# Performance work log

Measured on AMD Instinct MI355X. Metric: run time of the kernel, lower is better.

The kernel has to match this reference:

```python
import jax, jax.numpy as jnp
import numpy as np

ALPHA = 0.2  # LeakyReLU negative slope
NEG_INF = -9e15


def setup_inputs() -> dict:
    key = jax.random.key(0)
    k1, k2, k3, k4 = jax.random.split(key, 4)
    B, N, F_in, F_out = 8, 2048, 256, 128
    h = jax.random.normal(k1, (B, N, F_in), dtype=jnp.float32)
    adj = jax.random.randint(k2, (B, N, N), 0, 2, dtype=jnp.int32)
    # xavier_uniform with gain=1.414
    def xavier(k, shape, gain=1.414):
        fan_in, fan_out = shape[0], shape[1]
        limit = gain * np.sqrt(6.0 / (fan_in + fan_out))
        return jax.random.uniform(k, shape, jnp.float32, -limit, limit)
    W = xavier(k3, (F_in, F_out))
    a = xavier(k4, (2 * F_out, 1))
    return {"h": h, "adj": adj, "W": W, "a": a}


def reference(h, adj, W, a):
    # h: [B,N,F_in], adj: [B,N,N], W: [F_in,F_out], a: [2*F_out,1]
    Wh = jnp.einsum('bnf,fe->bne', h, W)  # [B,N,E]
    E = Wh.shape[-1]
    a_src, a_dst = a[:E, 0], a[E:, 0]
    # e[b,i,j] = leakyrelu(Wh[b,i].a_src + Wh[b,j].a_dst)  (additive decomposition
    # of a @ concat(Wh_i, Wh_j) -- same math, no [B,N,N,2E] intermediate)
    s_src = Wh @ a_src  # [B,N]
    s_dst = Wh @ a_dst  # [B,N]
    e = jax.nn.leaky_relu(s_src[:, :, None] + s_dst[:, None, :], negative_slope=ALPHA)
    e = jnp.where(adj > 0, e, NEG_INF)
    attention = jax.nn.softmax(e, axis=2)  # [B,N,N]
    # dropout p=0.0 / eval mode -> identity
    h_prime = jnp.einsum('bij,bje->bie', attention, Wh)
    return jax.nn.elu(h_prime)  # concat=True
```

## Files before the change

kernel.cpp:

```cpp
#include <hip/hip_runtime.h>
#include <hip/hip_bf16.h>

#define GAT_ALPHA 0.2f
#define LOG2E 1.4426950408889634f

typedef float f32x4 __attribute__((ext_vector_type(4)));
typedef int   i32x4 __attribute__((ext_vector_type(4)));
typedef short bf16x8 __attribute__((ext_vector_type(8)));

static constexpr int Nn  = 2048;
static constexpr int FIN = 256;
static constexpr int FO  = 128;

static __device__ __forceinline__ unsigned short f2bf(float x) {
    __hip_bfloat16 h = __float2bfloat16(x);
    return __builtin_bit_cast(unsigned short, h);
}
static __device__ __forceinline__ float bf2f(unsigned short u) {
    unsigned int v = ((unsigned int)u) << 16;
    return __builtin_bit_cast(float, v);
}

__global__ __launch_bounds__(256) void gat_prep(
        const float* __restrict__ W, const float* __restrict__ a,
        float* __restrict__ wa, unsigned int* __restrict__ md_key)
{
    __shared__ float pr[32][8];
    __shared__ float pd[32][8];
    const int t = threadIdx.x;
    const int kl = t >> 3, seg = t & 7;
    const int k = blockIdx.x * 32 + kl;
    float ps = 0.f, pv = 0.f;
    const float* wr = W + (size_t)k * FO + seg * 16;
    #pragma unroll
    for (int f = 0; f < 16; f += 4) {
        f32x4 wv = *(const f32x4*)(wr + f);
        f32x4 as = *(const f32x4*)(a + seg * 16 + f);
        f32x4 ad = *(const f32x4*)(a + FO + seg * 16 + f);
        ps += wv[0]*as[0] + wv[1]*as[1] + wv[2]*as[2] + wv[3]*as[3];
        pv += wv[0]*ad[0] + wv[1]*ad[1] + wv[2]*ad[2] + wv[3]*ad[3];
    }
    pr[kl][seg] = ps; pd[kl][seg] = pv;
    __syncthreads();
    if (t < 32) {
        float s = 0.f, d = 0.f;
        #pragma unroll
        for (int j = 0; j < 8; ++j) { s += pr[t][j]; d += pd[t][j]; }
        wa[blockIdx.x * 32 + t]       = s;
        wa[256 + blockIdx.x * 32 + t] = d;
    }
    if (blockIdx.x == 0 && t < 8) md_key[t] = 0u;
}

__global__ __launch_bounds__(256) void gat_wh(
        const float* __restrict__ h, const float* __restrict__ W,
        const float* __restrict__ wa, unsigned short* __restrict__ Wp,
        float* __restrict__ s_src, float* __restrict__ s_dst,
        unsigned int* __restrict__ md_key)
{
    __shared__ unsigned short WT[FO][264];
    __shared__ float wal[512];
    __shared__ float sred[64][4][2];
    __shared__ float red64[64];
    const int t  = threadIdx.x;
    const int b  = blockIdx.x & 7;
    const int n0 = (blockIdx.x >> 3) << 6;

    if (t < 128) *(f32x4*)&wal[t * 4] = *(const f32x4*)&wa[t * 4];
    #pragma unroll
    for (int c = 0; c < 32; ++c) {
        int flat = c * 1024 + t * 4;
        int k = flat >> 7, f = flat & 127;
        f32x4 wv = *(const f32x4*)&W[flat];
        WT[f + 0][k] = f2bf(wv[0]);
        WT[f + 1][k] = f2bf(wv[1]);
        WT[f + 2][k] = f2bf(wv[2]);
        WT[f + 3][k] = f2bf(wv[3]);
    }
    __syncthreads();

    {
        const int row = t >> 2, seg = t & 3;
        const float* hp  = h + ((size_t)(b * Nn + n0 + row)) * FIN + seg * 64;
        const float* was = &wal[seg * 64];
        const float* wad = &wal[256 + seg * 64];
        float ps = 0.f, pv = 0.f;
        #pragma unroll
        for (int j = 0; j < 64; j += 4) {
            f32x4 hv = *(const f32x4*)(hp + j);
            f32x4 sv = *(const f32x4*)(was + j);
            f32x4 dv = *(const f32x4*)(wad + j);
            ps += hv[0]*sv[0] + hv[1]*sv[1] + hv[2]*sv[2] + hv[3]*sv[3];
            pv += hv[0]*dv[0] + hv[1]*dv[1] + hv[2]*dv[2] + hv[3]*dv[3];
        }
        sred[row][seg][0] = ps;
        sred[row][seg][1] = pv;
    }
    __syncthreads();
    if (t < 64) {
        float s = sred[t][0][0] + sred[t][1][0] + sred[t][2][0] + sred[t][3][0];
        float d = sred[t][0][1] + sred[t][1][1] + sred[t][2][1] + sred[t][3][1];
        s_src[b * Nn + n0 + t] = s;
        s_dst[b * Nn + n0 + t] = d;
        red64[t] = d;
    }
    __syncthreads();
    if (t < 16) red64[t] = fmaxf(fmaxf(red64[t], red64[t + 16]),
                                 fmaxf(red64[t + 32], red64[t + 48]));
    __syncthreads();
    if (t == 0) {
        float m = red64[0];
        #pragma unroll
        for (int j = 1; j < 16; ++j) m = fmaxf(m, red64[j]);
        unsigned int bits = __builtin_bit_cast(unsigned int, m);
        unsigned int key  = (bits & 0x80000000u) ? ~bits : (bits | 0x80000000u);
        atomicMax(md_key + b, key);
    }

    const int w = t >> 6, lane = t & 63, n16 = lane & 15, quad = lane >> 4;
    const float* ha = h + ((size_t)(b * Nn + n0 + w * 16 + n16)) * FIN + quad * 8;
    f32x4 acc[8] = {};
    #pragma unroll
    for (int ks = 0; ks < 8; ++ks) {
        f32x4 h0 = *(const f32x4*)(ha + ks * 32);
        f32x4 h1 = *(const f32x4*)(ha + ks * 32 + 4);
        bf16x8 af;
        af[0] = (short)f2bf(h0[0]); af[1] = (short)f2bf(h0[1]);
        af[2] = (short)f2bf(h0[2]); af[3] = (short)f2bf(h0[3]);
        af[4] = (short)f2bf(h1[0]); af[5] = (short)f2bf(h1[1]);
        af[6] = (short)f2bf(h1[2]); af[7] = (short)f2bf(h1[3]);
        #pragma unroll
        for (int nt = 0; nt < 8; ++nt) {
            bf16x8 bfr = *(const bf16x8*)&WT[nt * 16 + n16][ks * 32 + quad * 8];
            acc[nt] = __builtin_amdgcn_mfma_f32_16x16x32_bf16(af, bfr, acc[nt], 0, 0, 0);
        }
    }
    {
        const int v      = (n0 >> 5) + (w >> 1);
        const int quad_p = ((w & 1) << 1) + (quad >> 1);
        const int eoff   = (quad & 1) << 2;
        #pragma unroll
        for (int nt = 0; nt < 8; ++nt) {
            ushort4 pk;
            pk.x = f2bf(acc[nt][0]); pk.y = f2bf(acc[nt][1]);
            pk.z = f2bf(acc[nt][2]); pk.w = f2bf(acc[nt][3]);
            size_t idx = ((((size_t)(b << 6) + v) * 8 + nt) * 64 + quad_p * 16 + n16) * 8 + eoff;
            *(ushort4*)&Wp[idx] = pk;
        }
    }
}

__global__ __launch_bounds__(512, 2) void gat_attn(
        const int* __restrict__ adj, const unsigned short* __restrict__ Wp,
        const float* __restrict__ s_src, const float* __restrict__ s_dst,
        const unsigned int* __restrict__ md_key, float* __restrict__ out)
{
    constexpr int AS = 132;
    __shared__ __align__(16) float smem_f[64 * AS];
    __shared__ float l_red[64];
    unsigned short* ldsw = (unsigned short*)smem_f;

    const int t = threadIdx.x, w = t >> 6, lane = t & 63;
    const int n16 = lane & 15, quad = lane >> 4;
    const int rg = w & 3, jwin = w >> 2;
    const int b  = blockIdx.x & 7;
    const int i0 = (blockIdx.x >> 3) << 6;

    if (t < 64) l_red[t] = 0.f;

    const unsigned int key = md_key[b];
    const unsigned int mb  = (key & 0x80000000u) ? (key ^ 0x80000000u) : ~key;
    const float mdb = __builtin_bit_cast(float, mb);

    const int row = i0 + rg * 16 + n16;
    const float ssr = s_src[b * Nn + row];
    const float tm  = ssr + mdb;
    const float mi  = fmaxf(tm, GAT_ALPHA * tm) * LOG2E;
    const float sL  = ssr * LOG2E;

    const int jw = (jwin << 5) + (quad << 3);
    const int* ap    = adj + ((size_t)(b * Nn + row)) * Nn + jw;
    const float* dptr = s_dst + b * Nn + jw;
    const unsigned short* wsrc = Wp + ((size_t)b << 18) + (t << 4);

    f32x4 acc[8] = {};
    float ls = 0.f;

    {
        f32x4 g0 = *(const f32x4*)(wsrc);
        f32x4 g1 = *(const f32x4*)(wsrc + 8);
        *(f32x4*)&ldsw[(t << 4)]     = g0;
        *(f32x4*)&ldsw[(t << 4) + 8] = g1;
    }
    i32x4 pa0 = *(const i32x4*)(ap);
    i32x4 pa1 = *(const i32x4*)(ap + 4);
    __syncthreads();

    for (int s = 0; s < 32; ++s) {
        const int j0  = s << 6;
        const int cur = s & 1, nxt = cur ^ 1;
        f32x4 d0 = *(const f32x4*)(dptr + j0);
        f32x4 d1 = *(const f32x4*)(dptr + j0 + 4);
        f32x4 g0, g1;
        if (s < 31) {
            const unsigned short* src = wsrc + (s + 1) * 8192;
            g0 = *(const f32x4*)(src);
            g1 = *(const f32x4*)(src + 8);
        }
        const int jn = (s < 31) ? ((s + 1) << 6) : 0;
        i32x4 na0 = *(const i32x4*)(ap + jn);
        i32x4 na1 = *(const i32x4*)(ap + jn + 4);

        bf16x8 af;
        #pragma unroll
        for (int j = 0; j < 4; ++j) {
            float u  = __builtin_fmaf(d0[j], LOG2E, sL);
            float lr = fmaxf(u, GAT_ALPHA * u);
            float e  = __builtin_amdgcn_exp2f(lr - mi);
            e = (pa0[j] > 0) ? e : 0.f;
            unsigned short us = f2bf(e);
            ls += bf2f(us); af[j] = (short)us;
        }
        #pragma unroll
        for (int j = 0; j < 4; ++j) {
            float u  = __builtin_fmaf(d1[j], LOG2E, sL);
            float lr = fmaxf(u, GAT_ALPHA * u);
            float e  = __builtin_amdgcn_exp2f(lr - mi);
            e = (pa1[j] > 0) ? e : 0.f;
            unsigned short us = f2bf(e);
            ls += bf2f(us); af[4 + j] = (short)us;
        }

        const unsigned short* bbase = &ldsw[cur * 8192 + (jwin << 12) + (lane << 3)];
        #pragma unroll
        for (int nt = 0; nt < 8; ++nt) {
            bf16x8 bfr = *(const bf16x8*)(bbase + (nt << 9));
            acc[nt] = __builtin_amdgcn_mfma_f32_16x16x32_bf16(af, bfr, acc[nt], 0, 0, 0);
        }

        if (s < 31) {
            *(f32x4*)&ldsw[nxt * 8192 + (t << 4)]     = g0;
            *(f32x4*)&ldsw[nxt * 8192 + (t << 4) + 8] = g1;
        }
        pa0 = na0; pa1 = na1;
        __syncthreads();
    }

    ls += __shfl_xor(ls, 16); ls += __shfl_xor(ls, 32);
    if (quad == 0) atomicAdd(&l_red[rg * 16 + n16], ls);

    float* slotp = smem_f + (size_t)(rg * 16) * AS;
    if (jwin == 0) {
        #pragma unroll
        for (int nt = 0; nt < 8; ++nt)
            #pragma unroll
            for (int rr = 0; rr < 4; ++rr)
                slotp[(quad * 4 + rr) * AS + nt * 16 + n16] = acc[nt][rr];
    }
    __syncthreads();
    if (jwin == 1) {
        #pragma unroll
        for (int nt = 0; nt < 8; ++nt)
            #pragma unroll
            for (int rr = 0; rr < 4; ++rr)
                slotp[(quad * 4 + rr) * AS + nt * 16 + n16] += acc[nt][rr];
    }
    __syncthreads();

    float* ob = out + ((size_t)(b * Nn + i0)) * FO;
    #pragma unroll
    for (int c = 0; c < 4; ++c) {
        int flat = c * 2048 + t * 4;
        int m = flat >> 7, f = flat & 127;
        f32x4 v = *(const f32x4*)&smem_f[(size_t)m * AS + f];
        float l = l_red[m];
        f32x4 o;
        #pragma unroll
        for (int j = 0; j < 4; ++j) {
            float x = v[j] / l;
            o[j] = x > 0.f ? x : expm1f(x);
        }
        *(f32x4*)&ob[(size_t)m * FO + f] = o;
    }
}

extern "C" void kernel_launch(void* const* d_in, const int* in_sizes, int n_in,
                              void* d_out, int out_size, void* d_ws, size_t ws_size,
                              hipStream_t stream)
{
    const float* h   = (const float*)d_in[0];
    const int*   adj = (const int*)d_in[1];
    const float* W   = (const float*)d_in[2];
    const float* a   = (const float*)d_in[3];
    float* out = (float*)d_out;

    char* ws = (char*)d_ws;
    unsigned short* Wp  = (unsigned short*)ws;
    float* s_src        = (float*)(ws + 4194304);
    float* s_dst        = (float*)(ws + 4259840);
    float* wa           = (float*)(ws + 4325376);
    unsigned int* md_key= (unsigned int*)(ws + 4327424);

    hipLaunchKernelGGL(gat_prep, dim3(8),   dim3(256), 0, stream, W, a, wa, md_key);
    hipLaunchKernelGGL(gat_wh,   dim3(256), dim3(256), 0, stream, h, W, wa, Wp, s_src, s_dst, md_key);
    hipLaunchKernelGGL(gat_attn, dim3(256), dim3(512), 0, stream, adj, Wp, s_src, s_dst, md_key, out);
}
```

Before: 256.3 us.

## Pack adjacency into bitmask in a separate kernel and stage mask and s_dst in LDS

Adds a gat_pack kernel that reads the int32 adjacency matrix in coalesced, row-contiguous order and uses wave ballots to pack it into a 1-bit-per-edge mask. The attention kernel then loads its 64 rows of mask words and the whole s_dst vector into LDS once per block, instead of streaming 32-bit adjacency values and s_dst from global memory inside the main loop. The aim is to take the large adjacency read off the MFMA loop's critical path and let it run at full bandwidth in a simple streaming kernel. The cost is an extra launch, a 4 MB mask write and read, and about 25 KB more LDS per block, which could limit occupancy.

```diff
diff --git a/kernel.cpp b/kernel.cpp
--- a/kernel.cpp
+++ b/kernel.cpp
@@ -50,6 +50,23 @@
         wa[256 + blockIdx.x * 32 + t] = d;
     }
     if (blockIdx.x == 0 && t < 8) md_key[t] = 0u;
+}
+
+__global__ __launch_bounds__(256) void gat_pack(
+        const int* __restrict__ adj, unsigned int* __restrict__ mask)
+{
+    const int t = threadIdx.x, lane = t & 63, w = t >> 6;
+    const size_t ibase = ((size_t)blockIdx.x * 4 + w) * 2048;
+    const int* src = adj + ibase + lane;
+    unsigned int myword = 0;
+    #pragma unroll
+    for (int c = 0; c < 32; ++c) {
+        int v = src[(size_t)c * 64];
+        unsigned long long m = __ballot(v > 0);
+        if (lane == 2 * c)     myword = (unsigned int)m;
+        if (lane == 2 * c + 1) myword = (unsigned int)(m >> 32);
+    }
+    mask[ibase / 32 + lane] = myword;
 }
 
 __global__ __launch_bounds__(256) void gat_wh(
@@ -151,12 +168,15 @@
 }
 
 __global__ __launch_bounds__(512, 2) void gat_attn(
-        const int* __restrict__ adj, const unsigned short* __restrict__ Wp,
+        const unsigned int* __restrict__ mask, const unsigned short* __restrict__ Wp,
         const float* __restrict__ s_src, const float* __restrict__ s_dst,
         const unsigned int* __restrict__ md_key, float* __restrict__ out)
 {
     constexpr int AS = 132;
+    constexpr int MS = 68;
     __shared__ __align__(16) float smem_f[64 * AS];
+    __shared__ __align__(16) unsigned int mlds[64 * MS];
+    __shared__ __align__(16) float dlds[Nn];
     __shared__ float l_red[64];
     unsigned short* ldsw = (unsigned short*)smem_f;
 
@@ -168,6 +188,19 @@
 
     if (t < 64) l_red[t] = 0.f;
 
+    {
+        const unsigned int* msrc = mask + ((size_t)(b * Nn + i0)) * 64 + t * 8;
+        i32x4 m0 = *(const i32x4*)(msrc);
+        i32x4 m1 = *(const i32x4*)(msrc + 4);
+        const int r = t >> 3, wd = (t & 7) * 8;
+        *(i32x4*)&mlds[r * MS + wd]     = m0;
+        *(i32x4*)&mlds[r * MS + wd + 4] = m1;
+    }
+    {
+        f32x4 dv = *(const f32x4*)(s_dst + b * Nn + t * 4);
+        *(f32x4*)&dlds[t * 4] = dv;
+    }
+
     const unsigned int key = md_key[b];
     const unsigned int mb  = (key & 0x80000000u) ? (key ^ 0x80000000u) : ~key;
     const float mdb = __builtin_bit_cast(float, mb);
@@ -179,8 +212,7 @@
     const float sL  = ssr * LOG2E;
 
     const int jw = (jwin << 5) + (quad << 3);
-    const int* ap    = adj + ((size_t)(b * Nn + row)) * Nn + jw;
-    const float* dptr = s_dst + b * Nn + jw;
+    const int mrow = (rg * 16 + n16) * MS;
     const unsigned short* wsrc = Wp + ((size_t)b << 18) + (t << 4);
 
     f32x4 acc[8] = {};
@@ -192,24 +224,21 @@
         *(f32x4*)&ldsw[(t << 4)]     = g0;
         *(f32x4*)&ldsw[(t << 4) + 8] = g1;
     }
-    i32x4 pa0 = *(const i32x4*)(ap);
-    i32x4 pa1 = *(const i32x4*)(ap + 4);
     __syncthreads();
 
     for (int s = 0; s < 32; ++s) {
         const int j0  = s << 6;
         const int cur = s & 1, nxt = cur ^ 1;
-        f32x4 d0 = *(const f32x4*)(dptr + j0);
-        f32x4 d1 = *(const f32x4*)(dptr + j0 + 4);
+        const unsigned int mword = mlds[mrow + s * 2 + jwin];
+        const unsigned int mbyte = (mword >> (quad * 8)) & 0xffu;
+        f32x4 d0 = *(const f32x4*)&dlds[j0 + jw];
+        f32x4 d1 = *(const f32x4*)&dlds[j0 + jw + 4];
         f32x4 g0, g1;
         if (s < 31) {
-            const unsigned short* src = wsrc + (s + 1) * 8192;
+            const unsigned short* src = wsrc + (size_t)(s + 1) * 8192;
             g0 = *(const f32x4*)(src);
             g1 = *(const f32x4*)(src + 8);
         }
-        const int jn = (s < 31) ? ((s + 1) << 6) : 0;
-        i32x4 na0 = *(const i32x4*)(ap + jn);
-        i32x4 na1 = *(const i32x4*)(ap + jn + 4);
 
         bf16x8 af;
         #pragma unroll
@@ -217,7 +246,7 @@
             float u  = __builtin_fmaf(d0[j], LOG2E, sL);
             float lr = fmaxf(u, GAT_ALPHA * u);
             float e  = __builtin_amdgcn_exp2f(lr - mi);
-            e = (pa0[j] > 0) ? e : 0.f;
+            e = ((mbyte >> j) & 1u) ? e : 0.f;
             unsigned short us = f2bf(e);
             ls += bf2f(us); af[j] = (short)us;
         }
@@ -226,7 +255,7 @@
             float u  = __builtin_fmaf(d1[j], LOG2E, sL);
             float lr = fmaxf(u, GAT_ALPHA * u);
             float e  = __builtin_amdgcn_exp2f(lr - mi);
-            e = (pa1[j] > 0) ? e : 0.f;
+            e = ((mbyte >> (4 + j)) & 1u) ? e : 0.f;
             unsigned short us = f2bf(e);
             ls += bf2f(us); af[4 + j] = (short)us;
         }
@@ -242,7 +271,6 @@
             *(f32x4*)&ldsw[nxt * 8192 + (t << 4)]     = g0;
             *(f32x4*)&ldsw[nxt * 8192 + (t << 4) + 8] = g1;
         }
-        pa0 = na0; pa1 = na1;
         __syncthreads();
     }
 
@@ -300,8 +328,10 @@
     float* s_dst        = (float*)(ws + 4259840);
     float* wa           = (float*)(ws + 4325376);
     unsigned int* md_key= (unsigned int*)(ws + 4327424);
-
-    hipLaunchKernelGGL(gat_prep, dim3(8),   dim3(256), 0, stream, W, a, wa, md_key);
-    hipLaunchKernelGGL(gat_wh,   dim3(256), dim3(256), 0, stream, h, W, wa, Wp, s_src, s_dst, md_key);
-    hipLaunchKernelGGL(gat_attn, dim3(256), dim3(512), 0, stream, adj, Wp, s_src, s_dst, md_key, out);
-}
+    unsigned int* mask  = (unsigned int*)(ws + 8388608);
+
+    hipLaunchKernelGGL(gat_prep, dim3(8),    dim3(256), 0, stream, W, a, wa, md_key);
+    hipLaunchKernelGGL(gat_wh,   dim3(256),  dim3(256), 0, stream, h, W, wa, Wp, s_src, s_dst, md_key);
+    hipLaunchKernelGGL(gat_pack, dim3(4096), dim3(256), 0, stream, adj, mask);
+    hipLaunchKernelGGL(gat_attn, dim3(256),  dim3(512), 0, stream, mask, Wp, s_src, s_dst, md_key, out);
+}
```

New measurement: 247.5 us. 3.5% less time.

## Pack adjacency into LDS bitmasks via ballot with coalesced prefetch pipeline

Applied to the files above, without the earlier changes.

Adjacency is now loaded coalesced, one row per wave with lanes spanning columns, and packed into 32-bit bitmasks in LDS via __ballot. Those masks are prefetched several tiles ahead, and s_dst is staged once in LDS. The aim is to replace strided per-thread int4 adjacency reads with coalesced ones and to deepen prefetch to hide the dominant HBM traffic of the int32 adj matrix. The cost is extra LDS (mask and s_dst buffers), which may reduce occupancy, plus ballot and LDS write overhead each tile.

```diff
diff --git a/kernel.cpp b/kernel.cpp
--- a/kernel.cpp
+++ b/kernel.cpp
@@ -156,7 +156,10 @@
         const unsigned int* __restrict__ md_key, float* __restrict__ out)
 {
     constexpr int AS = 132;
+    constexpr int MS = 68;
     __shared__ __align__(16) float smem_f[64 * AS];
+    __shared__ __align__(16) unsigned int mlds[64 * MS];
+    __shared__ __align__(16) float dlds[Nn];
     __shared__ float l_red[64];
     unsigned short* ldsw = (unsigned short*)smem_f;
 
@@ -168,83 +171,119 @@
 
     if (t < 64) l_red[t] = 0.f;
 
+    const int* abase = adj + ((size_t)(b * Nn + i0 + w * 8)) * Nn + lane;
+    const unsigned short* wsrc = Wp + ((size_t)b << 18);
+
+    f32x4 pg0 = *(const f32x4*)(wsrc + t * 8);
+    f32x4 pg1 = *(const f32x4*)(wsrc + 4096 + t * 8);
+    int pv[16];
+    #pragma unroll
+    for (int k = 0; k < 16; ++k) {
+        const int rr = k & 7, c = k >> 3;
+        pv[k] = abase[(size_t)rr * Nn + (c << 6)];
+    }
+    int avQ[8], avP[8];
+    #pragma unroll
+    for (int rr = 0; rr < 8; ++rr) avQ[rr] = abase[(size_t)rr * Nn + 128];
+    *(f32x4*)&dlds[t * 4] = *(const f32x4*)(s_dst + b * Nn + t * 4);
+
     const unsigned int key = md_key[b];
     const unsigned int mb  = (key & 0x80000000u) ? (key ^ 0x80000000u) : ~key;
     const float mdb = __builtin_bit_cast(float, mb);
-
     const int row = i0 + rg * 16 + n16;
     const float ssr = s_src[b * Nn + row];
     const float tm  = ssr + mdb;
     const float mi  = fmaxf(tm, GAT_ALPHA * tm) * LOG2E;
     const float sL  = ssr * LOG2E;
-
-    const int jw = (jwin << 5) + (quad << 3);
-    const int* ap    = adj + ((size_t)(b * Nn + row)) * Nn + jw;
-    const float* dptr = s_dst + b * Nn + jw;
-    const unsigned short* wsrc = Wp + ((size_t)b << 18) + (t << 4);
+    const int jw   = (jwin << 5) + (quad << 3);
+    const int mrow = (rg * 16 + n16) * MS;
+
+    #pragma unroll
+    for (int k = 0; k < 16; ++k) {
+        const int rr = k & 7, c = k >> 3;
+        unsigned long long m = __ballot(pv[k] > 0);
+        if (lane == 0) mlds[(w * 8 + rr) * MS + (c << 1)]     = (unsigned int)m;
+        if (lane == 1) mlds[(w * 8 + rr) * MS + (c << 1) + 1] = (unsigned int)(m >> 32);
+    }
+    *(f32x4*)&ldsw[t * 8]        = pg0;
+    *(f32x4*)&ldsw[4096 + t * 8] = pg1;
 
     f32x4 acc[8] = {};
     float ls = 0.f;
-
-    {
-        f32x4 g0 = *(const f32x4*)(wsrc);
-        f32x4 g1 = *(const f32x4*)(wsrc + 8);
-        *(f32x4*)&ldsw[(t << 4)]     = g0;
-        *(f32x4*)&ldsw[(t << 4) + 8] = g1;
-    }
-    i32x4 pa0 = *(const i32x4*)(ap);
-    i32x4 pa1 = *(const i32x4*)(ap + 4);
-    __syncthreads();
-
-    for (int s = 0; s < 32; ++s) {
-        const int j0  = s << 6;
-        const int cur = s & 1, nxt = cur ^ 1;
-        f32x4 d0 = *(const f32x4*)(dptr + j0);
-        f32x4 d1 = *(const f32x4*)(dptr + j0 + 4);
-        f32x4 g0, g1;
-        if (s < 31) {
-            const unsigned short* src = wsrc + (s + 1) * 8192;
-            g0 = *(const f32x4*)(src);
-            g1 = *(const f32x4*)(src + 8);
-        }
-        const int jn = (s < 31) ? ((s + 1) << 6) : 0;
-        i32x4 na0 = *(const i32x4*)(ap + jn);
-        i32x4 na1 = *(const i32x4*)(ap + jn + 4);
-
-        bf16x8 af;
-        #pragma unroll
-        for (int j = 0; j < 4; ++j) {
-            float u  = __builtin_fmaf(d0[j], LOG2E, sL);
-            float lr = fmaxf(u, GAT_ALPHA * u);
-            float e  = __builtin_amdgcn_exp2f(lr - mi);
-            e = (pa0[j] > 0) ? e : 0.f;
-            unsigned short us = f2bf(e);
-            ls += bf2f(us); af[j] = (short)us;
-        }
-        #pragma unroll
-        for (int j = 0; j < 4; ++j) {
-            float u  = __builtin_fmaf(d1[j], LOG2E, sL);
-            float lr = fmaxf(u, GAT_ALPHA * u);
-            float e  = __builtin_amdgcn_exp2f(lr - mi);
-            e = (pa1[j] > 0) ? e : 0.f;
-            unsigned short us = f2bf(e);
-            ls += bf2f(us); af[4 + j] = (short)us;
-        }
-
-        const unsigned short* bbase = &ldsw[cur * 8192 + (jwin << 12) + (lane << 3)];
-        #pragma unroll
-        for (int nt = 0; nt < 8; ++nt) {
-            bf16x8 bfr = *(const bf16x8*)(bbase + (nt << 9));
-            acc[nt] = __builtin_amdgcn_mfma_f32_16x16x32_bf16(af, bfr, acc[nt], 0, 0, 0);
-        }
-
-        if (s < 31) {
-            *(f32x4*)&ldsw[nxt * 8192 + (t << 4)]     = g0;
-            *(f32x4*)&ldsw[nxt * 8192 + (t << 4) + 8] = g1;
-        }
-        pa0 = na0; pa1 = na1;
-        __syncthreads();
-    }
+    __syncthreads();
+
+#define GAT_TILE(S, CUR, AV_ISSUE, AV_BALLOT)                                   \
+    {                                                                           \
+        const int s_ = (S);                                                     \
+        const int j0_ = s_ << 6;                                                \
+        const unsigned int mword = mlds[mrow + (s_ << 1) + jwin];               \
+        const unsigned int mbyte = (mword >> (quad * 8)) & 0xffu;               \
+        f32x4 d0 = *(const f32x4*)&dlds[j0_ + jw];                              \
+        f32x4 d1 = *(const f32x4*)&dlds[j0_ + jw + 4];                          \
+                           \
+        if (s_ < 29) {                                                          \
+            const int off_ = (s_ + 3) << 6;                                     \
+            _Pragma("unroll")                                                   \
+            for (int rr = 0; rr < 8; ++rr)                                      \
+                AV_ISSUE[rr] = abase[(size_t)rr * Nn + off_];                   \
+        }                                                                       \
+                                               \
+        f32x4 g0, g1;                                                           \
+        if (s_ < 31) {                                                          \
+            const unsigned short* src_ = wsrc + (size_t)(s_ + 1) * 8192;        \
+            g0 = *(const f32x4*)(src_ + t * 8);                                 \
+            g1 = *(const f32x4*)(src_ + 4096 + t * 8);                          \
+        }                                                                       \
+                                                         \
+        bf16x8 af;                                                              \
+        _Pragma("unroll")                                                       \
+        for (int j = 0; j < 4; ++j) {                                           \
+            float u  = __builtin_fmaf(d0[j], LOG2E, sL);                        \
+            float lr = fmaxf(u, GAT_ALPHA * u);                                 \
+            float e  = __builtin_amdgcn_exp2f(lr - mi);                         \
+            e = ((mbyte >> j) & 1u) ? e : 0.f;                                  \
+            unsigned short us = f2bf(e);                                        \
+            ls += bf2f(us); af[j] = (short)us;                                  \
+        }                                                                       \
+        _Pragma("unroll")                                                       \
+        for (int j = 0; j < 4; ++j) {                                           \
+            float u  = __builtin_fmaf(d1[j], LOG2E, sL);                        \
+            float lr = fmaxf(u, GAT_ALPHA * u);                                 \
+            float e  = __builtin_amdgcn_exp2f(lr - mi);                         \
+            e = ((mbyte >> (4 + j)) & 1u) ? e : 0.f;                            \
+            unsigned short us = f2bf(e);                                        \
+            ls += bf2f(us); af[4 + j] = (short)us;                              \
+        }                                                                       \
+                                               \
+        const unsigned short* bbase = &ldsw[(CUR) * 8192 + (jwin << 12) + (lane << 3)]; \
+        _Pragma("unroll")                                                       \
+        for (int nt = 0; nt < 8; ++nt) {                                        \
+            bf16x8 bfr = *(const bf16x8*)(bbase + (nt << 9));                   \
+            acc[nt] = __builtin_amdgcn_mfma_f32_16x16x32_bf16(af, bfr, acc[nt], 0, 0, 0); \
+        }                                                                       \
+                    \
+        if (s_ < 30) {                                                          \
+            const int cw_ = (s_ + 2) << 1;                                      \
+            _Pragma("unroll")                                                   \
+            for (int rr = 0; rr < 8; ++rr) {                                    \
+                unsigned long long m = __ballot(AV_BALLOT[rr] > 0);             \
+                if (lane == 0) mlds[(w * 8 + rr) * MS + cw_]     = (unsigned int)m; \
+                if (lane == 1) mlds[(w * 8 + rr) * MS + cw_ + 1] = (unsigned int)(m >> 32); \
+            }                                                                   \
+        }                                                                       \
+                     \
+        if (s_ < 31) {                                                          \
+            *(f32x4*)&ldsw[((CUR) ^ 1) * 8192 + t * 8]        = g0;             \
+            *(f32x4*)&ldsw[((CUR) ^ 1) * 8192 + 4096 + t * 8] = g1;             \
+        }                                                                       \
+        __syncthreads();                                                        \
+    }
+
+    for (int s = 0; s < 32; s += 2) {
+        GAT_TILE(s,     0, avP, avQ)
+        GAT_TILE(s + 1, 1, avQ, avP)
+    }
+#undef GAT_TILE
 
     ls += __shfl_xor(ls, 16); ls += __shfl_xor(ls, 32);
     if (quad == 0) atomicAdd(&l_red[rg * 16 + n16], ls);
```

Result: faster. 236.1 us (-7.9%).
